# Kernel tuning notes

Measured on AMD Instinct MI355X. Metric: run time of the kernel, lower is better.

Reference implementation:

```python
import jax, jax.numpy as jnp
import numpy as np

B, C, IN_H, IN_W = 32, 16, 64, 64
OUT_H, OUT_W, K, STRIDE = 60, 60, 5, 1


def setup_inputs() -> dict:
    key = jax.random.key(0)
    k1, k2 = jax.random.split(key)
    # spike-like inputs in [0,1)
    in_spikes = jax.random.uniform(k1, (B, C, IN_H, IN_W), dtype=jnp.float32)
    # unshared locally-connected weights: (outH, outW, C_in, K, K, C_out)
    weights = jax.random.normal(k2, (OUT_H, OUT_W, C, K, K, C), dtype=jnp.float32) * (1.0 / (K * K))
    return {"in_spikes": in_spikes, "weights": weights}


def _extract_patches(x, out_h, out_w, k, stride):
    # x: (B, C, H, W) -> patches: (B, C, K, K, out_h, out_w)
    # static K*K loop over kernel offsets (not a data-dim loop)
    rows = []
    for di in range(k):
        cols = []
        for dj in range(k):
            cols.append(x[:, :, di:di + out_h * stride:stride, dj:dj + out_w * stride:stride])
        rows.append(jnp.stack(cols, axis=2))  # (B, C, K, out_h, out_w)
    return jnp.stack(rows, axis=2)  # (B, C, K, K, out_h, out_w)


def reference(in_spikes, weights):
    out_h, out_w, _, k, _, _ = weights.shape
    patches = _extract_patches(in_spikes, out_h, out_w, k, STRIDE)
    # output[b, k_out, i, j] = sum_{c,u,v} patches[b,c,u,v,i,j] * weights[i,j,c,u,v,k_out]
    out = jnp.einsum('bcuvij,ijcuvk->bkij', patches, weights)
    return out
```

## Files before the change

kernel.cpp:

```cpp
#include <hip/hip_runtime.h>
#include <hip/hip_bf16.h>


#define OUT_HW 60
#define IN_HW  64
#define CIN    16
#define COUT   16
#define NPOS   3600
#define BK     512
#define XC_ELE (32u * 64u * 64u * 16u)

typedef __attribute__((ext_vector_type(8))) short bf16x8;
typedef __attribute__((ext_vector_type(4))) float f32x4;

static __device__ __forceinline__ unsigned pk2(float a, float b) {
    union { __hip_bfloat162 h; unsigned u; } cv;
    cv.h = __float22bfloat162_rn(make_float2(a, b));
    return cv.u;
}

static __device__ __forceinline__ void g2lds16(const float* g, float* l) {
    __builtin_amdgcn_global_load_lds(
        (const __attribute__((address_space(1))) unsigned int*)g,
        (__attribute__((address_space(3))) unsigned int*)l, 16, 0, 0);
}

__global__ __launch_bounds__(256)
void make_xc(const float* __restrict__ x, ushort* __restrict__ xc) {
    const int bh = blockIdx.x;
    const int b = bh >> 6, h = bh & 63;
    const int t = threadIdx.x;
    const int cq = t & 3, wc = t >> 2;
    const float* src = x + ((size_t)(b * CIN) * IN_HW + h) * IN_HW + wc;
    float f[4];
#pragma unroll
    for (int e = 0; e < 4; ++e)
        f[e] = src[(size_t)(cq * 4 + e) * (IN_HW * IN_HW)];
    union { ushort4 v; unsigned u[2]; } o;
    o.u[0] = pk2(f[0], f[1]);
    o.u[1] = pk2(f[2], f[3]);
    *(ushort4*)&xc[((size_t)bh * IN_HW + wc) * CIN + cq * 4] = o.v;
}

template<int PACKED>
__global__ __launch_bounds__(256, 4)
void lc_pos(const ushort* __restrict__ xc, const float* __restrict__ w,
            float* __restrict__ dst) {
    __shared__ float sWraw[6400] __attribute__((aligned(16)));
    __shared__ float sRed[4][32 * 17];

    const int bid = blockIdx.x;
    const int pos = (bid & 7) * 450 + (bid >> 3);
    const int i = pos / OUT_HW, j = pos - i * OUT_HW;
    const int t = threadIdx.x;
    const int lane = t & 63, wv = t >> 6;
    const int l15 = lane & 15, q = lane >> 4;
    const int qh = q >> 1, c0 = (q & 1) << 3;

    const float* wsrc = w + (size_t)pos * 6400 + lane * 4;
    for (int o = wv; o < 25; o += 4)
        g2lds16(wsrc + o * 256, &sWraw[o * 256]);

    const int base_hw = i * IN_HW + j;
    bf16x8 xa0[4], xa1[4];
#pragma unroll
    for (int it = 0; it < 4; ++it) {
        const int cc = wv + it * 4;
        if (cc < 13) {
            const int uvB = cc * 2 + qh;
            const int uvA = (uvB < 25) ? uvB : 24;
            const int uA = (uvA * 13) >> 6;
            const int vA = uvA - 5 * uA;
            const size_t xoff = (size_t)l15 * (IN_HW * IN_HW * CIN)
                              + (size_t)(base_hw + uA * IN_HW + vA) * CIN + c0;
            xa0[it] = *(const bf16x8*)(xc + xoff);
            xa1[it] = *(const bf16x8*)(xc + xoff + 16u * IN_HW * IN_HW * CIN);
        }
    }

    __syncthreads();

    f32x4 acc0 = {0.f, 0.f, 0.f, 0.f}, acc1 = {0.f, 0.f, 0.f, 0.f};
#pragma unroll
    for (int it = 0; it < 4; ++it) {
        const int cc = wv + it * 4;
        if (cc < 13) {
            const int uvB = cc * 2 + qh;
            const int okB = (uvB < 25);
            float bfv[8];
#pragma unroll
            for (int jj = 0; jj < 8; ++jj)
                bfv[jj] = okB ? sWraw[(c0 + jj) * 400 + uvB * 16 + l15] : 0.f;
            union { bf16x8 v; unsigned u[4]; } pb;
#pragma unroll
            for (int jj = 0; jj < 4; ++jj) pb.u[jj] = pk2(bfv[2 * jj], bfv[2 * jj + 1]);
            acc0 = __builtin_amdgcn_mfma_f32_16x16x32_bf16(xa0[it], pb.v, acc0, 0, 0, 0);
            acc1 = __builtin_amdgcn_mfma_f32_16x16x32_bf16(xa1[it], pb.v, acc1, 0, 0, 0);
        }
    }

#pragma unroll
    for (int r = 0; r < 4; ++r) {
        sRed[wv][(q * 4 + r) * 17 + l15]      = acc0[r];
        sRed[wv][(q * 4 + r + 16) * 17 + l15] = acc1[r];
    }
    __syncthreads();
#pragma unroll
    for (int h = 0; h < 2; ++h) {
        const int o = t + h * 256;
        const int idx = (o >> 4) * 17 + (o & 15);
        const float sv = sRed[0][idx] + sRed[1][idx] + sRed[2][idx] + sRed[3][idx];
        if (PACKED) dst[(size_t)pos * BK + o] = sv;
        else        dst[(size_t)o * NPOS + pos] = sv;
    }
}

__global__ __launch_bounds__(256)
void transpose_out(const float* __restrict__ src, float* __restrict__ out) {
    __shared__ float tile[64][65];
    const int o0 = blockIdx.x * 64;
    const int k0 = blockIdx.y * 64;
    const int t  = threadIdx.x;
    const int tx = t & 63, ty = t >> 6;
    for (int r = ty; r < 64; r += 4) {
        const int oij = o0 + r;
        if (oij < NPOS) tile[r][tx] = src[(size_t)oij * BK + k0 + tx];
    }
    __syncthreads();
    for (int r = ty; r < 64; r += 4) {
        const int oij = o0 + tx;
        if (oij < NPOS) out[(size_t)(k0 + r) * NPOS + oij] = tile[tx][r];
    }
}

__global__ __launch_bounds__(256)
void lc_naive(const float* __restrict__ x, const float* __restrict__ w,
              float* __restrict__ out) {
    const int gid = blockIdx.x * 256 + threadIdx.x;
    if (gid >= 32 * COUT * NPOS) return;
    const int j = gid % OUT_HW;
    int rest = gid / OUT_HW;
    const int i = rest % OUT_HW; rest /= OUT_HW;
    const int k = rest % COUT;
    const int b = rest / COUT;
    const float* wp = w + (size_t)(i * OUT_HW + j) * 6400 + k;
    float s = 0.f;
    for (int c = 0; c < CIN; ++c)
        for (int u = 0; u < 5; ++u)
            for (int v = 0; v < 5; ++v)
                s += x[((size_t)(b * CIN + c) * IN_HW + i + u) * IN_HW + j + v]
                   * wp[((c * 5 + u) * 5 + v) * COUT];
    out[gid] = s;
}

extern "C" void kernel_launch(void* const* d_in, const int* in_sizes, int n_in,
                              void* d_out, int out_size, void* d_ws, size_t ws_size,
                              hipStream_t stream) {
    const float* x = (const float*)d_in[0];
    const float* w = (const float*)d_in[1];
    float* out = (float*)d_out;

    const size_t xcBytes  = (size_t)XC_ELE * 2;
    const size_t outBytes = (size_t)NPOS * BK * 4;
    ushort* xc = (ushort*)d_ws;

    if (ws_size >= xcBytes + outBytes) {
        float* wsOut = (float*)((char*)d_ws + xcBytes);
        make_xc<<<32 * IN_HW, 256, 0, stream>>>(x, xc);
        lc_pos<1><<<NPOS, 256, 0, stream>>>(xc, w, wsOut);
        transpose_out<<<dim3((NPOS + 63) / 64, BK / 64), 256, 0, stream>>>(wsOut, out);
    } else if (ws_size >= xcBytes) {
        make_xc<<<32 * IN_HW, 256, 0, stream>>>(x, xc);
        lc_pos<0><<<NPOS, 256, 0, stream>>>(xc, w, out);
    } else {
        lc_naive<<<(32 * COUT * NPOS + 255) / 256, 256, 0, stream>>>(x, w, out);
    }
}
```

Before: 155.1 us.

## Split lc_pos work by batch half per wave, removing cross-wave K reduction

The per-position kernel now uses two waves, each owning 16 batch rows and iterating over the full reduction of 13 chunks, instead of four waves splitting the reduction dimension. This removes the shared-memory partial-sum buffer, the second barrier and the four-way reduction. In exchange each wave does more serial MFMAs and holds 13 preloaded A fragments in registers, and fewer threads per block issue the weight copy.

Measured after the change: 157.6 us. About the same (+1.6%).

```diff
diff --git a/kernel.cpp b/kernel.cpp
--- a/kernel.cpp
+++ b/kernel.cpp
@@ -43,11 +43,10 @@
 }
 
 template<int PACKED>
-__global__ __launch_bounds__(256, 4)
+__global__ __launch_bounds__(128, 3)
 void lc_pos(const ushort* __restrict__ xc, const float* __restrict__ w,
             float* __restrict__ dst) {
     __shared__ float sWraw[6400] __attribute__((aligned(16)));
-    __shared__ float sRed[4][32 * 17];
 
     const int bid = blockIdx.x;
     const int pos = (bid & 7) * 450 + (bid >> 3);
@@ -58,60 +57,44 @@
     const int qh = q >> 1, c0 = (q & 1) << 3;
 
     const float* wsrc = w + (size_t)pos * 6400 + lane * 4;
-    for (int o = wv; o < 25; o += 4)
+    for (int o = wv; o < 25; o += 2)
         g2lds16(wsrc + o * 256, &sWraw[o * 256]);
 
     const int base_hw = i * IN_HW + j;
-    bf16x8 xa0[4], xa1[4];
+    const size_t bofs = (size_t)(wv * 16 + l15) * (IN_HW * IN_HW * CIN);
+    bf16x8 xa[13];
 #pragma unroll
-    for (int it = 0; it < 4; ++it) {
-        const int cc = wv + it * 4;
-        if (cc < 13) {
-            const int uvB = cc * 2 + qh;
-            const int uvA = (uvB < 25) ? uvB : 24;
-            const int uA = (uvA * 13) >> 6;
-            const int vA = uvA - 5 * uA;
-            const size_t xoff = (size_t)l15 * (IN_HW * IN_HW * CIN)
-                              + (size_t)(base_hw + uA * IN_HW + vA) * CIN + c0;
-            xa0[it] = *(const bf16x8*)(xc + xoff);
-            xa1[it] = *(const bf16x8*)(xc + xoff + 16u * IN_HW * IN_HW * CIN);
-        }
+    for (int cc = 0; cc < 13; ++cc) {
+        const int uvB = cc * 2 + qh;
+        const int uvA = (uvB < 25) ? uvB : 24;
+        const int uA = (uvA * 13) >> 6;
+        const int vA = uvA - 5 * uA;
+        xa[cc] = *(const bf16x8*)(xc + bofs
+                   + (size_t)(base_hw + uA * IN_HW + vA) * CIN + c0);
     }
 
     __syncthreads();
 
-    f32x4 acc0 = {0.f, 0.f, 0.f, 0.f}, acc1 = {0.f, 0.f, 0.f, 0.f};
+    f32x4 acc = {0.f, 0.f, 0.f, 0.f};
 #pragma unroll
-    for (int it = 0; it < 4; ++it) {
-        const int cc = wv + it * 4;
-        if (cc < 13) {
-            const int uvB = cc * 2 + qh;
-            const int okB = (uvB < 25);
-            float bfv[8];
+    for (int cc = 0; cc < 13; ++cc) {
+        const int uvB = cc * 2 + qh;
+        const int okB = (uvB < 25);
+        float bfv[8];
 #pragma unroll
-            for (int jj = 0; jj < 8; ++jj)
-                bfv[jj] = okB ? sWraw[(c0 + jj) * 400 + uvB * 16 + l15] : 0.f;
-            union { bf16x8 v; unsigned u[4]; } pb;
+        for (int jj = 0; jj < 8; ++jj)
+            bfv[jj] = okB ? sWraw[(c0 + jj) * 400 + uvB * 16 + l15] : 0.f;
+        union { bf16x8 v; unsigned u[4]; } pb;
 #pragma unroll
-            for (int jj = 0; jj < 4; ++jj) pb.u[jj] = pk2(bfv[2 * jj], bfv[2 * jj + 1]);
-            acc0 = __builtin_amdgcn_mfma_f32_16x16x32_bf16(xa0[it], pb.v, acc0, 0, 0, 0);
-            acc1 = __builtin_amdgcn_mfma_f32_16x16x32_bf16(xa1[it], pb.v, acc1, 0, 0, 0);
-        }
+        for (int jj = 0; jj < 4; ++jj) pb.u[jj] = pk2(bfv[2 * jj], bfv[2 * jj + 1]);
+        acc = __builtin_amdgcn_mfma_f32_16x16x32_bf16(xa[cc], pb.v, acc, 0, 0, 0);
     }
 
 #pragma unroll
     for (int r = 0; r < 4; ++r) {
-        sRed[wv][(q * 4 + r) * 17 + l15]      = acc0[r];
-        sRed[wv][(q * 4 + r + 16) * 17 + l15] = acc1[r];
-    }
-    __syncthreads();
-#pragma unroll
-    for (int h = 0; h < 2; ++h) {
-        const int o = t + h * 256;
-        const int idx = (o >> 4) * 17 + (o & 15);
-        const float sv = sRed[0][idx] + sRed[1][idx] + sRed[2][idx] + sRed[3][idx];
-        if (PACKED) dst[(size_t)pos * BK + o] = sv;
-        else        dst[(size_t)o * NPOS + pos] = sv;
+        const int o = (wv * 16 + q * 4 + r) * 16 + l15;
+        if (PACKED) dst[(size_t)pos * BK + o] = acc[r];
+        else        dst[(size_t)o * NPOS + pos] = acc[r];
     }
 }
 
@@ -167,11 +150,11 @@
     if (ws_size >= xcBytes + outBytes) {
         float* wsOut = (float*)((char*)d_ws + xcBytes);
         make_xc<<<32 * IN_HW, 256, 0, stream>>>(x, xc);
-        lc_pos<1><<<NPOS, 256, 0, stream>>>(xc, w, wsOut);
+        lc_pos<1><<<NPOS, 128, 0, stream>>>(xc, w, wsOut);
         transpose_out<<<dim3((NPOS + 63) / 64, BK / 64), 256, 0, stream>>>(wsOut, out);
     } else if (ws_size >= xcBytes) {
         make_xc<<<32 * IN_HW, 256, 0, stream>>>(x, xc);
-        lc_pos<0><<<NPOS, 256, 0, stream>>>(xc, w, out);
+        lc_pos<0><<<NPOS, 128, 0, stream>>>(xc, w, out);
     } else {
         lc_naive<<<(32 * COUT * NPOS + 255) / 256, 256, 0, stream>>>(x, w, out);
     }
```

## Reorder bf16 input staging to HW-major, batch-inner layout for contiguous gathers

Applied to the files above, without the earlier changes.

Changes the staged bf16 input from a (B,H,W,C) layout to (H,W,B,C), so the 32 batch rows of each spatial location sit contiguously. In the per-position MFMA kernel, the 16 lanes that load different batches now read adjacent 32-byte chunks instead of addresses 128 KB apart, which should improve coalescing and cache-line use. The conversion kernel now runs only 64 blocks, each thread handling 8 batches and 16 channels, so that stage has much less parallelism and may take longer.

Result: slower. 159.8 us (+3.0%).

```diff
diff --git a/kernel.cpp b/kernel.cpp
--- a/kernel.cpp
+++ b/kernel.cpp
@@ -8,7 +8,8 @@
 #define COUT   16
 #define NPOS   3600
 #define BK     512
-#define XC_ELE (32u * 64u * 64u * 16u)
+#define HWSTR  512
+#define XC_ELE (64u * 64u * 32u * 16u)
 
 typedef __attribute__((ext_vector_type(8))) short bf16x8;
 typedef __attribute__((ext_vector_type(4))) float f32x4;
@@ -26,25 +27,31 @@
 }
 
 __global__ __launch_bounds__(256)
-void make_xc(const float* __restrict__ x, ushort* __restrict__ xc) {
-    const int bh = blockIdx.x;
-    const int b = bh >> 6, h = bh & 63;
+void make_xc2(const float* __restrict__ x, ushort* __restrict__ xc2) {
+    const int h = blockIdx.x;
     const int t = threadIdx.x;
-    const int cq = t & 3, wc = t >> 2;
-    const float* src = x + ((size_t)(b * CIN) * IN_HW + h) * IN_HW + wc;
-    float f[4];
+    const int wj = t & 63;
 #pragma unroll
-    for (int e = 0; e < 4; ++e)
-        f[e] = src[(size_t)(cq * 4 + e) * (IN_HW * IN_HW)];
-    union { ushort4 v; unsigned u[2]; } o;
-    o.u[0] = pk2(f[0], f[1]);
-    o.u[1] = pk2(f[2], f[3]);
-    *(ushort4*)&xc[((size_t)bh * IN_HW + wc) * CIN + cq * 4] = o.v;
+    for (int it = 0; it < 8; ++it) {
+        const int b = (t >> 6) + it * 4;
+        const float* src = x + ((size_t)(b * CIN) * IN_HW + h) * IN_HW + wj;
+        float f[16];
+#pragma unroll
+        for (int c = 0; c < 16; ++c)
+            f[c] = src[(size_t)c * (IN_HW * IN_HW)];
+        union { ushort v[16]; uint4 u[2]; } o;
+#pragma unroll
+        for (int e = 0; e < 8; ++e)
+            ((unsigned*)o.v)[e] = pk2(f[2 * e], f[2 * e + 1]);
+        uint4* dst = (uint4*)&xc2[((size_t)(h * IN_HW + wj) * 32 + b) * 16];
+        dst[0] = o.u[0];
+        dst[1] = o.u[1];
+    }
 }
 
 template<int PACKED>
 __global__ __launch_bounds__(256, 4)
-void lc_pos(const ushort* __restrict__ xc, const float* __restrict__ w,
+void lc_pos(const ushort* __restrict__ xc2, const float* __restrict__ w,
             float* __restrict__ dst) {
     __shared__ float sWraw[6400] __attribute__((aligned(16)));
     __shared__ float sRed[4][32 * 17];
@@ -71,10 +78,10 @@
             const int uvA = (uvB < 25) ? uvB : 24;
             const int uA = (uvA * 13) >> 6;
             const int vA = uvA - 5 * uA;
-            const size_t xoff = (size_t)l15 * (IN_HW * IN_HW * CIN)
-                              + (size_t)(base_hw + uA * IN_HW + vA) * CIN + c0;
-            xa0[it] = *(const bf16x8*)(xc + xoff);
-            xa1[it] = *(const bf16x8*)(xc + xoff + 16u * IN_HW * IN_HW * CIN);
+            const ushort* p = xc2
+                + (size_t)(base_hw + uA * IN_HW + vA) * HWSTR + l15 * 16 + c0;
+            xa0[it] = *(const bf16x8*)(p);
+            xa1[it] = *(const bf16x8*)(p + 256);
         }
     }
 
@@ -162,16 +169,16 @@
 
     const size_t xcBytes  = (size_t)XC_ELE * 2;
     const size_t outBytes = (size_t)NPOS * BK * 4;
-    ushort* xc = (ushort*)d_ws;
+    ushort* xc2 = (ushort*)d_ws;
 
     if (ws_size >= xcBytes + outBytes) {
         float* wsOut = (float*)((char*)d_ws + xcBytes);
-        make_xc<<<32 * IN_HW, 256, 0, stream>>>(x, xc);
-        lc_pos<1><<<NPOS, 256, 0, stream>>>(xc, w, wsOut);
+        make_xc2<<<IN_HW, 256, 0, stream>>>(x, xc2);
+        lc_pos<1><<<NPOS, 256, 0, stream>>>(xc2, w, wsOut);
         transpose_out<<<dim3((NPOS + 63) / 64, BK / 64), 256, 0, stream>>>(wsOut, out);
     } else if (ws_size >= xcBytes) {
-        make_xc<<<32 * IN_HW, 256, 0, stream>>>(x, xc);
-        lc_pos<0><<<NPOS, 256, 0, stream>>>(xc, w, out);
+        make_xc2<<<IN_HW, 256, 0, stream>>>(x, xc2);
+        lc_pos<0><<<NPOS, 256, 0, stream>>>(xc2, w, out);
     } else {
         lc_naive<<<(32 * COUT * NPOS + 255) / 256, 256, 0, stream>>>(x, w, out);
     }
```
